# Optimization experiments

Measured on AMD Instinct MI355X. Metric: run time of the kernel, lower is better.

The kernel has to match this reference:

```python
import jax, jax.numpy as jnp
import numpy as np

EPS = 0.1  # label smoothing eps (paper page 8)
B, C, V = 4, 2048, 32000


def setup_inputs() -> dict:
    key = jax.random.key(0)
    k1, k2, k3 = jax.random.split(key, 3)
    dec_input = jax.random.randint(k1, (B, C), 0, V)                  # token ids, 'bc'
    dec_output = jax.random.normal(k2, (B, C, V), dtype=jnp.float32)  # logits, 'bct'
    token_histo = jax.random.uniform(k3, (V,), dtype=jnp.float32) + 1e-3
    return {"dec_input": dec_input, "dec_output": dec_output, "token_histo": token_histo}


def reference(dec_input, dec_output, token_histo):
    # unigram distribution used for smoothing
    u = token_histo / token_histo.sum()                    # (V,)
    labels = dec_input[:, 1:]                              # (B, C-1) shifted targets
    logits = dec_output[:, :-1, :]                         # (B, C-1, V) predictions
    logp = jax.nn.log_softmax(logits, axis=-1)             # single stable pass
    # soft-target CE: -(1-eps)*logp[label] - eps*sum_v u[v]*logp[v]
    nll = -jnp.take_along_axis(logp, labels[..., None], axis=-1)[..., 0]  # (B, C-1)
    smooth = -jnp.einsum('bcv,v->bc', logp, u)             # (B, C-1)
    xent = (1.0 - EPS) * nll + EPS * smooth
    return jnp.mean(xent)  # F.cross_entropy default mean reduction
```

## Files before the change

kernel.cpp:

```cpp
#include <hip/hip_runtime.h>
#include <math.h>

#define BB 4
#define CC 2048
#define VV 32000
#define ROWS (BB * (CC - 1))
#define EPSF 0.1f

typedef float f32x4 __attribute__((ext_vector_type(4)));

__global__ __launch_bounds__(256) void row_xent_kernel(
    const int* __restrict__ dec_input,
    const float* __restrict__ dec_output,
    const float* __restrict__ histo,
    float* __restrict__ row_out) {
  const int row = blockIdx.x;
  const int b = row / (CC - 1);
  const int c = row % (CC - 1);
  const float* __restrict__ x = dec_output + ((size_t)b * CC + c) * VV;
  const int tid = threadIdx.x;

  float m0 = -INFINITY, s0 = 0.0f, d0 = 0.0f;
  float m1 = -INFINITY, s1 = 0.0f, d1 = 0.0f;
  float hs = 0.0f;

  const f32x4* __restrict__ x4 = (const f32x4*)x;
  const f32x4* __restrict__ h4 = (const f32x4*)histo;

#define CHUNK(I, M, S, D)                                              \
  {                                                                    \
    f32x4 xv = __builtin_nontemporal_load(&x4[I]);                     \
    f32x4 hv = h4[I];                                                  \
    D = fmaf(xv.x, hv.x, D);                                           \
    D = fmaf(xv.y, hv.y, D);                                           \
    D = fmaf(xv.z, hv.z, D);                                           \
    D = fmaf(xv.w, hv.w, D);                                           \
    hs += (hv.x + hv.y) + (hv.z + hv.w);                               \
    float lm = fmaxf(fmaxf(xv.x, xv.y), fmaxf(xv.z, xv.w));            \
    float nm = fmaxf(M, lm);                                           \
    S = S * __expf(M - nm)                                             \
        + __expf(xv.x - nm) + __expf(xv.y - nm)                        \
        + __expf(xv.z - nm) + __expf(xv.w - nm);                       \
    M = nm;                                                            \
  }

  int i = tid;
  for (; i + 256 < VV / 4; i += 512) {
    CHUNK(i, m0, s0, d0);
    CHUNK(i + 256, m1, s1, d1);
  }
  if (i < VV / 4) CHUNK(i, m0, s0, d0);
#undef CHUNK

  float m = fmaxf(m0, m1);
  float s = s0 * __expf(m0 - m) + s1 * __expf(m1 - m);
  float dot = d0 + d1;

  for (int off = 1; off < 64; off <<= 1) {
    float om = __shfl_xor(m, off);
    float os = __shfl_xor(s, off);
    float od = __shfl_xor(dot, off);
    float oh = __shfl_xor(hs, off);
    float nm = fmaxf(m, om);
    s = s * __expf(m - nm) + os * __expf(om - nm);
    m = nm;
    dot += od;
    hs += oh;
  }

  __shared__ float sm_m[4], sm_s[4], sm_d[4], sm_h[4];
  const int wave = tid >> 6;
  if ((tid & 63) == 0) { sm_m[wave] = m; sm_s[wave] = s; sm_d[wave] = dot; sm_h[wave] = hs; }
  __syncthreads();
  if (tid == 0) {
    float M = sm_m[0], Sx = sm_s[0], D = sm_d[0], H = sm_h[0];
    #pragma unroll
    for (int w = 1; w < 4; ++w) {
      float nm = fmaxf(M, sm_m[w]);
      Sx = Sx * __expf(M - nm) + sm_s[w] * __expf(sm_m[w] - nm);
      M = nm;
      D += sm_d[w];
      H += sm_h[w];
    }
    const float lse = M + __logf(Sx);
    const int label = dec_input[b * CC + c + 1];
    const float xl = x[label];
    row_out[row] = lse - (1.0f - EPSF) * xl - EPSF * (D / H);
  }
}

__global__ __launch_bounds__(256) void final_mean_kernel(
    const float* __restrict__ row_out, float* __restrict__ out) {
  __shared__ float sm[256];
  int tid = threadIdx.x;
  float s = 0.0f;
  const f32x4* __restrict__ r4 = (const f32x4*)row_out;
  for (int i = tid; i < ROWS / 4; i += 256) {
    f32x4 v = r4[i];
    s += (v.x + v.y) + (v.z + v.w);
  }
  sm[tid] = s;
  __syncthreads();
  for (int off = 128; off > 0; off >>= 1) {
    if (tid < off) sm[tid] += sm[tid + off];
    __syncthreads();
  }
  if (tid == 0) out[0] = sm[0] * (1.0f / (float)ROWS);
}

extern "C" void kernel_launch(void* const* d_in, const int* in_sizes, int n_in,
                              void* d_out, int out_size, void* d_ws, size_t ws_size,
                              hipStream_t stream) {
  const int*   dec_input  = (const int*)d_in[0];
  const float* dec_output = (const float*)d_in[1];
  const float* histo      = (const float*)d_in[2];
  float* out = (float*)d_out;
  float* ws  = (float*)d_ws;

  row_xent_kernel<<<ROWS, 256, 0, stream>>>(dec_input, dec_output, histo, ws);
  final_mean_kernel<<<1, 256, 0, stream>>>(ws, out);
}
```

Before: 182.3 us.

## Fuse mean reduction via fixed-point atomics and widen per-thread accumulators to four

Removes the separate final-mean kernel. Each block quantizes its row loss to 32.32 fixed point and atomically adds it to a 64-bit accumulator, and the last block (found through an atomic counter) writes the mean. The main loop also unrolls to four independent online-softmax accumulator sets to expose more memory-level parallelism. In exchange it adds a memset launch, global atomics, a small fixed-point quantization error, and extra registers per thread.

```diff
diff --git a/kernel.cpp b/kernel.cpp
--- a/kernel.cpp
+++ b/kernel.cpp
@@ -6,6 +6,7 @@
 #define VV 32000
 #define ROWS (BB * (CC - 1))
 #define EPSF 0.1f
+#define NV4 (VV / 4)
 
 typedef float f32x4 __attribute__((ext_vector_type(4)));
 
@@ -13,7 +14,9 @@
     const int* __restrict__ dec_input,
     const float* __restrict__ dec_output,
     const float* __restrict__ histo,
-    float* __restrict__ row_out) {
+    unsigned long long* __restrict__ acc,
+    unsigned int* __restrict__ cnt,
+    float* __restrict__ out) {
   const int row = blockIdx.x;
   const int b = row / (CC - 1);
   const int c = row % (CC - 1);
@@ -22,6 +25,8 @@
 
   float m0 = -INFINITY, s0 = 0.0f, d0 = 0.0f;
   float m1 = -INFINITY, s1 = 0.0f, d1 = 0.0f;
+  float m2 = -INFINITY, s2 = 0.0f, d2 = 0.0f;
+  float m3 = -INFINITY, s3 = 0.0f, d3 = 0.0f;
   float hs = 0.0f;
 
   const f32x4* __restrict__ x4 = (const f32x4*)x;
@@ -45,16 +50,22 @@
   }
 
   int i = tid;
-  for (; i + 256 < VV / 4; i += 512) {
-    CHUNK(i, m0, s0, d0);
+  for (; i + 768 < NV4; i += 1024) {
+    CHUNK(i,       m0, s0, d0);
     CHUNK(i + 256, m1, s1, d1);
+    CHUNK(i + 512, m2, s2, d2);
+    CHUNK(i + 768, m3, s3, d3);
   }
-  if (i < VV / 4) CHUNK(i, m0, s0, d0);
+  for (; i < NV4; i += 256) CHUNK(i, m0, s0, d0);
 #undef CHUNK
 
-  float m = fmaxf(m0, m1);
-  float s = s0 * __expf(m0 - m) + s1 * __expf(m1 - m);
-  float dot = d0 + d1;
+  float ma = fmaxf(m0, m1);
+  float sa = s0 * __expf(m0 - ma) + s1 * __expf(m1 - ma);
+  float mb = fmaxf(m2, m3);
+  float sb = s2 * __expf(m2 - mb) + s3 * __expf(m3 - mb);
+  float m = fmaxf(ma, mb);
+  float s = sa * __expf(ma - m) + sb * __expf(mb - m);
+  float dot = (d0 + d1) + (d2 + d3);
 
   for (int off = 1; off < 64; off <<= 1) {
     float om = __shfl_xor(m, off);
@@ -85,27 +96,19 @@
     const float lse = M + __logf(Sx);
     const int label = dec_input[b * CC + c + 1];
     const float xl = x[label];
-    row_out[row] = lse - (1.0f - EPSF) * xl - EPSF * (D / H);
+    const float xent = lse - (1.0f - EPSF) * xl - EPSF * (D / H);
+
+    long long q = llrintf(xent * 4294967296.0f);
+    atomicAdd(acc, (unsigned long long)q);
+    __threadfence();
+    unsigned int prev = atomicAdd(cnt, 1u);
+    if (prev == ROWS - 1) {
+      __threadfence();
+      unsigned long long total = atomicAdd(acc, 0ULL);
+      double sum = (double)(long long)total * (1.0 / 4294967296.0);
+      out[0] = (float)(sum / (double)ROWS);
+    }
   }
-}
-
-__global__ __launch_bounds__(256) void final_mean_kernel(
-    const float* __restrict__ row_out, float* __restrict__ out) {
-  __shared__ float sm[256];
-  int tid = threadIdx.x;
-  float s = 0.0f;
-  const f32x4* __restrict__ r4 = (const f32x4*)row_out;
-  for (int i = tid; i < ROWS / 4; i += 256) {
-    f32x4 v = r4[i];
-    s += (v.x + v.y) + (v.z + v.w);
-  }
-  sm[tid] = s;
-  __syncthreads();
-  for (int off = 128; off > 0; off >>= 1) {
-    if (tid < off) sm[tid] += sm[tid + off];
-    __syncthreads();
-  }
-  if (tid == 0) out[0] = sm[0] * (1.0f / (float)ROWS);
 }
 
 extern "C" void kernel_launch(void* const* d_in, const int* in_sizes, int n_in,
@@ -115,8 +118,10 @@
   const float* dec_output = (const float*)d_in[1];
   const float* histo      = (const float*)d_in[2];
   float* out = (float*)d_out;
-  float* ws  = (float*)d_ws;
+  unsigned long long* acc = (unsigned long long*)d_ws;
+  unsigned int* cnt = (unsigned int*)((char*)d_ws + 8);
 
-  row_xent_kernel<<<ROWS, 256, 0, stream>>>(dec_input, dec_output, histo, ws);
-  final_mean_kernel<<<1, 256, 0, stream>>>(ws, out);
+  hipMemsetAsync(d_ws, 0, 16, stream);
+  row_xent_kernel<<<ROWS, 256, 0, stream>>>(dec_input, dec_output, histo,
+                                            acc, cnt, out);
 }
```

Result: slower. 599.5 us (+228.7%).
